# Kernel tuning notes

Measured on AMD Instinct MI355X. Metric: run time of the kernel, lower is better.

Reference implementation:

```python
import jax, jax.numpy as jnp
import numpy as np

N_NODES = 100000
N_EDGES = 1600000
N_FEAT = 16
HIDDEN = 128
N_GRAPHS = 512


def setup_inputs() -> dict:
    key = jax.random.key(0)
    ks = jax.random.split(key, 9)
    x = jax.random.normal(ks[0], (N_NODES, N_FEAT), dtype=jnp.float32)
    edge_index = jax.random.randint(ks[1], (2, N_EDGES), 0, N_NODES, dtype=jnp.int64)
    batch = jnp.sort(jax.random.randint(ks[2], (N_NODES,), 0, N_GRAPHS, dtype=jnp.int64))
    s1 = 1.0 / np.sqrt(N_FEAT)
    s2 = 1.0 / np.sqrt(HIDDEN)
    W1 = jax.random.uniform(ks[3], (N_FEAT, HIDDEN), jnp.float32, -s1, s1)
    b1 = jax.random.uniform(ks[4], (HIDDEN,), jnp.float32, -s1, s1)
    W2 = jax.random.uniform(ks[5], (HIDDEN, HIDDEN), jnp.float32, -s2, s2)
    b2 = jax.random.uniform(ks[6], (HIDDEN,), jnp.float32, -s2, s2)
    Wl = jax.random.uniform(ks[7], (HIDDEN, 1), jnp.float32, -s2, s2)
    bl = jax.random.uniform(ks[8], (1,), jnp.float32, -s2, s2)
    return {"x": x, "edge_index": edge_index, "batch": batch,
            "W1": W1, "b1": b1, "W2": W2, "b2": b2, "Wl": Wl, "bl": bl}


def _gcn_conv(x, W, b, src, dst, n_nodes):
    # PyG GCNConv: h = x @ W; add self-loops; sym-normalized scatter-add; + bias
    h = x @ W  # [N, H]
    deg = jnp.zeros((n_nodes,), h.dtype).at[dst].add(1.0) + 1.0  # self-loop adds 1
    dinv = jax.lax.rsqrt(deg)  # deg >= 1, safe
    norm = dinv[src] * dinv[dst]  # [E]
    out = jnp.zeros_like(h).at[dst].add(h[src] * norm[:, None])
    out = out + h * (dinv * dinv)[:, None]  # self-loop term
    return out + b


def reference(x, edge_index, batch, W1, b1, W2, b2, Wl, bl):
    src, dst = edge_index[0], edge_index[1]
    n = x.shape[0]
    h = jax.nn.relu(_gcn_conv(x, W1, b1, src, dst, n))
    h = jax.nn.relu(_gcn_conv(h, W2, b2, src, dst, n))
    # global_mean_pool over graphs
    sums = jax.ops.segment_sum(h, batch, num_segments=N_GRAPHS)
    counts = jax.ops.segment_sum(jnp.ones((n,), h.dtype), batch, num_segments=N_GRAPHS)
    pooled = sums / jnp.maximum(counts, 1.0)[:, None]  # [G, H]
    return (pooled @ Wl + bl).squeeze(-1)  # [G]
```

## Files before the change

kernel.cpp:

```cpp
#include <hip/hip_runtime.h>
#include <hip/hip_bf16.h>

#define N_NODES 100000
#define N_EDGES 1600000
#define N_FEAT  16
#define HIDDEN  128
#define N_GRAPHS 512
#define CAP     64
#define NBKT    782
#define BN      128
#define CAPB    2560
#define EPB     4000

typedef unsigned short ushort_t;
typedef short v8s __attribute__((ext_vector_type(8)));
typedef float v4f __attribute__((ext_vector_type(4)));

__device__ __forceinline__ ushort_t f2bf(float f) {
    __hip_bfloat16 b = __float2bfloat16(f);
    return *(ushort_t*)&b;
}
__device__ __forceinline__ float bf_lo(unsigned u) {
    union { unsigned i; float f; } c; c.i = u << 16; return c.f;
}
__device__ __forceinline__ float bf_hi(unsigned u) {
    union { unsigned i; float f; } c; c.i = u & 0xffff0000u; return c.f;
}


__global__ __launch_bounds__(256) void k_part(const int* __restrict__ src,
                                              const int* __restrict__ dst,
                                              int* __restrict__ bcnt,
                                              int* __restrict__ ebuf) {
    __shared__ int h[NBKT];
    __shared__ int base[NBKT];
    __shared__ int r[NBKT];
    int tid = threadIdx.x;
    int e0 = blockIdx.x * EPB;

    for (int i = tid; i < NBKT; i += 256) { h[i] = 0; r[i] = 0; }
    __syncthreads();

    int nloc = (tid < EPB - 15 * 256) ? 16 : 15;
    int v[16], bb[16];
    #pragma unroll
    for (int k = 0; k < 16; ++k) {
        if (k < nloc) {
            int i = e0 + tid + k * 256;
            int s = src[i], d = dst[i];
            bb[k] = d >> 7;
            v[k] = s | ((d & 127) << 17);
            atomicAdd(&h[bb[k]], 1);
        }
    }
    __syncthreads();

    for (int i = tid; i < NBKT; i += 256)
        base[i] = atomicAdd(&bcnt[i], h[i]);
    __syncthreads();

    #pragma unroll
    for (int k = 0; k < 16; ++k) {
        if (k < nloc) {
            int b = bb[k];
            int pos = base[b] + atomicAdd(&r[b], 1);
            if (pos < CAPB) ebuf[b * CAPB + pos] = v[k];
        }
    }
}


__global__ __launch_bounds__(256) void k_fill(const int* __restrict__ bcnt,
                                              const int* __restrict__ ebuf,
                                              int* __restrict__ esrc64,
                                              int* __restrict__ cnt,
                                              float* __restrict__ dinv) {
    __shared__ int lcnt[BN];
    int tid = threadIdx.x;
    int b = blockIdx.x;
    int node0 = b << 7;

    if (tid < BN) lcnt[tid] = 0;
    __syncthreads();

    int nE = bcnt[b]; nE = nE > CAPB ? CAPB : nE;
    const int* eb = ebuf + b * CAPB;
    for (int i = tid; i < nE; i += 256) {
        int v = eb[i];
        int dl = v >> 17;
        int p = atomicAdd(&lcnt[dl], 1);
        if (p < CAP) esrc64[((node0 + dl) << 6) + p] = v & 0x1FFFF;
    }
    __syncthreads();

    if (tid < BN) {
        int node = node0 + tid;
        if (node < N_NODES) {
            int c = lcnt[tid];
            cnt[node] = c;
            dinv[node] = rsqrtf((float)c + 1.0f);
            int cc = c > CAP ? CAP : c;
            int pad = (cc + 7) & ~7;
            for (int p = cc; p < pad; ++p)
                esrc64[(node << 6) + p] = N_NODES;
        }
    }
}


__global__ void k_prescale(const float* __restrict__ x, const float* __restrict__ dinv,
                           ushort_t* __restrict__ xb, ushort_t* __restrict__ h1) {
    int i = blockIdx.x * 256 + threadIdx.x;
    if (i < N_NODES * N_FEAT) {
        xb[i] = f2bf(x[i] * dinv[i >> 4]);
    } else if (i < (N_NODES + 1) * N_FEAT) {
        xb[i] = 0;
    } else if (i < (N_NODES + 1) * N_FEAT + HIDDEN) {
        h1[(size_t)N_NODES * HIDDEN + (i - (N_NODES + 1) * N_FEAT)] = 0;
    }
}


__global__ __launch_bounds__(256) void k_agg1f(const int* __restrict__ cnt,
                                               const int* __restrict__ esrc64,
                                               const float* __restrict__ dinv,
                                               const ushort_t* __restrict__ xb,
                                               const float* __restrict__ W1,
                                               const float* __restrict__ b1,
                                               ushort_t* __restrict__ h1) {
    __shared__ float sw[N_FEAT * HIDDEN];
    __shared__ float sx[32][20];
    __shared__ float sdd[32];
    int tid = threadIdx.x;
    for (int i = tid; i < N_FEAT * HIDDEN; i += 256) sw[i] = W1[i];

    int wv = tid >> 6;
    int sub = (tid >> 3) & 7;
    int l8 = tid & 7;
    int nl = wv * 8 + sub;
    int node = blockIdx.x * 32 + nl;
    const unsigned* xr = (const unsigned*)xb;

    int deg = cnt[node]; deg = deg > CAP ? CAP : deg;
    int deg8 = (deg + 7) & ~7;
    int base = node << 6;
    float dd = dinv[node];

    float a0 = 0.0f, a1 = 0.0f;
    for (int j = 0; j < deg8; j += 8) {
        int4 ia = *(const int4*)(esrc64 + base + j);
        int4 ib = *(const int4*)(esrc64 + base + j + 4);
        unsigned u0 = xr[(unsigned)ia.x * 8 + l8];
        unsigned u1 = xr[(unsigned)ia.y * 8 + l8];
        unsigned u2 = xr[(unsigned)ia.z * 8 + l8];
        unsigned u3 = xr[(unsigned)ia.w * 8 + l8];
        unsigned u4 = xr[(unsigned)ib.x * 8 + l8];
        unsigned u5 = xr[(unsigned)ib.y * 8 + l8];
        unsigned u6 = xr[(unsigned)ib.z * 8 + l8];
        unsigned u7 = xr[(unsigned)ib.w * 8 + l8];
        a0 += bf_lo(u0) + bf_lo(u1) + bf_lo(u2) + bf_lo(u3)
            + bf_lo(u4) + bf_lo(u5) + bf_lo(u6) + bf_lo(u7);
        a1 += bf_hi(u0) + bf_hi(u1) + bf_hi(u2) + bf_hi(u3)
            + bf_hi(u4) + bf_hi(u5) + bf_hi(u6) + bf_hi(u7);
    }
    unsigned su = xr[(unsigned)node * 8 + l8];
    a0 = (a0 + bf_lo(su)) * dd;
    a1 = (a1 + bf_hi(su)) * dd;

    sx[nl][2 * l8] = a0;
    sx[nl][2 * l8 + 1] = a1;
    if (l8 == 0) sdd[nl] = dd;
    __syncthreads();

    int f = tid & 127, half = tid >> 7;
    float bias = b1[f];
    float acc[16];
    #pragma unroll
    for (int n = 0; n < 16; ++n) acc[n] = bias;
    #pragma unroll
    for (int k4 = 0; k4 < 4; ++k4) {
        float w0 = sw[(k4 * 4 + 0) * HIDDEN + f];
        float w1 = sw[(k4 * 4 + 1) * HIDDEN + f];
        float w2 = sw[(k4 * 4 + 2) * HIDDEN + f];
        float w3 = sw[(k4 * 4 + 3) * HIDDEN + f];
        #pragma unroll
        for (int n = 0; n < 16; ++n) {
            float4 xv = *(const float4*)(&sx[half * 16 + n][k4 * 4]);
            acc[n] += xv.x * w0 + xv.y * w1 + xv.z * w2 + xv.w * w3;
        }
    }
    int n0 = blockIdx.x * 32 + half * 16;
    #pragma unroll
    for (int n = 0; n < 16; ++n)
        h1[(size_t)(n0 + n) * HIDDEN + f] =
            f2bf(sdd[half * 16 + n] * fmaxf(acc[n], 0.0f));
}


__global__ __launch_bounds__(256) void k_agg2(const int* __restrict__ cnt,
                                              const int* __restrict__ esrc64,
                                              const float* __restrict__ dinv,
                                              const ushort_t* __restrict__ h1,
                                              ushort_t* __restrict__ aggb) {
    int tid = threadIdx.x;
    int sub = tid >> 5;
    int l32 = tid & 31;
    int node = blockIdx.x * 8 + sub;
    const uint2* h = (const uint2*)h1;
    int deg = cnt[node]; deg = deg > CAP ? CAP : deg;
    int deg8 = (deg + 7) & ~7;
    int base = node << 6;
    float dd = dinv[node];

    uint2 sv = h[node * 32 + l32];
    float a0 = bf_lo(sv.x), a1 = bf_hi(sv.x), a2 = bf_lo(sv.y), a3 = bf_hi(sv.y);

    for (int j = 0; j < deg8; j += 8) {
        int4 ia = *(const int4*)(esrc64 + base + j);
        int4 ib = *(const int4*)(esrc64 + base + j + 4);
        uint2 v0 = h[(unsigned)ia.x * 32 + l32];
        uint2 v1 = h[(unsigned)ia.y * 32 + l32];
        uint2 v2 = h[(unsigned)ia.z * 32 + l32];
        uint2 v3 = h[(unsigned)ia.w * 32 + l32];
        uint2 v4 = h[(unsigned)ib.x * 32 + l32];
        uint2 v5 = h[(unsigned)ib.y * 32 + l32];
        uint2 v6 = h[(unsigned)ib.z * 32 + l32];
        uint2 v7 = h[(unsigned)ib.w * 32 + l32];
        a0 += bf_lo(v0.x) + bf_lo(v1.x) + bf_lo(v2.x) + bf_lo(v3.x)
            + bf_lo(v4.x) + bf_lo(v5.x) + bf_lo(v6.x) + bf_lo(v7.x);
        a1 += bf_hi(v0.x) + bf_hi(v1.x) + bf_hi(v2.x) + bf_hi(v3.x)
            + bf_hi(v4.x) + bf_hi(v5.x) + bf_hi(v6.x) + bf_hi(v7.x);
        a2 += bf_lo(v0.y) + bf_lo(v1.y) + bf_lo(v2.y) + bf_lo(v3.y)
            + bf_lo(v4.y) + bf_lo(v5.y) + bf_lo(v6.y) + bf_lo(v7.y);
        a3 += bf_hi(v0.y) + bf_hi(v1.y) + bf_hi(v2.y) + bf_hi(v3.y)
            + bf_hi(v4.y) + bf_hi(v5.y) + bf_hi(v6.y) + bf_hi(v7.y);
    }
    ushort4 r;
    r.x = f2bf(a0 * dd); r.y = f2bf(a1 * dd);
    r.z = f2bf(a2 * dd); r.w = f2bf(a3 * dd);
    ((ushort4*)aggb)[node * 32 + l32] = r;
}


__global__ void k_packB(const float* __restrict__ W2, ushort_t* __restrict__ Bp) {
    int idx = blockIdx.x * 256 + threadIdx.x;
    int j = idx & 7;
    int lane = (idx >> 3) & 63;
    int nt = (idx >> 9) & 7;
    int kt = idx >> 12;
    int k = kt * 32 + (lane >> 4) * 8 + j;
    int n = nt * 16 + (lane & 15);
    Bp[idx] = f2bf(W2[k * HIDDEN + n]);
}


__global__ __launch_bounds__(256) void k_mm2m(const ushort_t* __restrict__ A,
                                              const ushort_t* __restrict__ Bp,
                                              const float* __restrict__ b2,
                                              const float* __restrict__ Wl,
                                              float* __restrict__ snode) {
    __shared__ ushort_t sB[16384];
    int tid = threadIdx.x;
    {
        const uint4* s = (const uint4*)Bp;
        uint4* d = (uint4*)sB;
        #pragma unroll
        for (int j = 0; j < 8; ++j) d[tid + 256 * j] = s[tid + 256 * j];
    }
    __syncthreads();

    int wv = tid >> 6, lane = tid & 63;
    int m = lane & 15, quad = lane >> 4;
    int node0 = blockIdx.x * 64 + wv * 16;
    const ushort_t* arow = A + (size_t)(node0 + m) * HIDDEN;

    v4f acc[8];
    #pragma unroll
    for (int nt = 0; nt < 8; ++nt) acc[nt] = (v4f){0.f, 0.f, 0.f, 0.f};

    #pragma unroll
    for (int kt = 0; kt < 4; ++kt) {
        v8s a = *(const v8s*)(arow + kt * 32 + quad * 8);
        #pragma unroll
        for (int nt = 0; nt < 8; ++nt) {
            v8s b = *(const v8s*)(&sB[((kt * 8 + nt) * 64 + lane) * 8]);
            acc[nt] = __builtin_amdgcn_mfma_f32_16x16x32_bf16(a, b, acc[nt], 0, 0, 0);
        }
    }

    float part[4] = {0, 0, 0, 0};
    #pragma unroll
    for (int nt = 0; nt < 8; ++nt) {
        float bb = b2[nt * 16 + m];
        float wl = Wl[nt * 16 + m];
        #pragma unroll
        for (int reg = 0; reg < 4; ++reg)
            part[reg] += fmaxf(acc[nt][reg] + bb, 0.0f) * wl;
    }
    #pragma unroll
    for (int reg = 0; reg < 4; ++reg) {
        float p = part[reg];
        p += __shfl_xor(p, 1, 64);
        p += __shfl_xor(p, 2, 64);
        p += __shfl_xor(p, 4, 64);
        p += __shfl_xor(p, 8, 64);
        int node = node0 + quad * 4 + reg;
        if (m == 0 && node < N_NODES) snode[node] = p;
    }
}


__global__ __launch_bounds__(256) void k_pool(const float* __restrict__ snode,
                                              const int* __restrict__ batch,
                                              const float* __restrict__ bl,
                                              float* __restrict__ out) {
    int g = blockIdx.x;
    int tid = threadIdx.x;
    __shared__ float sred[4];

    int lo = 0, hi = N_NODES;
    while (lo < hi) { int mid = (lo + hi) >> 1; if (batch[mid] < g) lo = mid + 1; else hi = mid; }
    int start = lo;
    hi = N_NODES;
    while (lo < hi) { int mid = (lo + hi) >> 1; if (batch[mid] < g + 1) lo = mid + 1; else hi = mid; }
    int end = lo;

    float acc = 0.0f;
    for (int n = start + tid; n < end; n += 256) acc += snode[n];

    #pragma unroll
    for (int off = 32; off; off >>= 1) acc += __shfl_down(acc, off, 64);
    int wave = tid >> 6, lane = tid & 63;
    if (lane == 0) sred[wave] = acc;
    __syncthreads();
    if (tid == 0) {
        float s = sred[0] + sred[1] + sred[2] + sred[3];
        float cnt = (float)(end - start);
        out[g] = s / fmaxf(cnt, 1.0f) + bl[0];
    }
}


extern "C" void kernel_launch(void* const* d_in, const int* in_sizes, int n_in,
                              void* d_out, int out_size, void* d_ws, size_t ws_size,
                              hipStream_t stream) {
    const float* x    = (const float*)d_in[0];
    const int*   src  = (const int*)d_in[1];
    const int*   dst  = src + N_EDGES;
    const int*   batch= (const int*)d_in[2];
    const float* W1   = (const float*)d_in[3];
    const float* b1   = (const float*)d_in[4];
    const float* W2   = (const float*)d_in[5];
    const float* b2   = (const float*)d_in[6];
    const float* Wl   = (const float*)d_in[7];
    const float* bl   = (const float*)d_in[8];
    float* out = (float*)d_out;

    const size_t NH  = (size_t)N_NODES * HIDDEN;
    const size_t NH1 = (size_t)(N_NODES + 1) * HIDDEN;

    ushort_t* h1   = (ushort_t*)d_ws;
    ushort_t* aggb = h1 + NH1;
    int*   ebuf    = (int*)aggb;
    ushort_t* xb   = aggb + NH;
    float* dinv    = (float*)(xb + (size_t)(N_NODES + 1) * N_FEAT);
    float* snode   = dinv + N_NODES;
    int*   cnt     = (int*)(snode + N_NODES);
    int*   esrc64  = cnt + N_NODES;
    int*   bcnt    = esrc64 + (size_t)N_NODES * CAP;
    ushort_t* Bp   = (ushort_t*)(bcnt + NBKT);

    hipMemsetAsync(bcnt, 0, NBKT * sizeof(int), stream);
    k_part<<<N_EDGES / EPB, 256, 0, stream>>>(src, dst, bcnt, ebuf);
    k_fill<<<NBKT, 256, 0, stream>>>(bcnt, ebuf, esrc64, cnt, dinv);

    {
        int total = (N_NODES + 1) * N_FEAT + HIDDEN;
        k_prescale<<<(total + 255) / 256, 256, 0, stream>>>(x, dinv, xb, h1);
    }
    k_packB<<<64, 256, 0, stream>>>(W2, Bp);

    k_agg1f<<<N_NODES / 32, 256, 0, stream>>>(cnt, esrc64, dinv, xb, W1, b1, h1);

    k_agg2<<<N_NODES / 8, 256, 0, stream>>>(cnt, esrc64, dinv, h1, aggb);
    k_mm2m<<<(N_NODES + 63) / 64, 256, 0, stream>>>(aggb, Bp, b2, Wl, snode);

    k_pool<<<N_GRAPHS, 256, 0, stream>>>(snode, batch, bl, out);
}
```

Measured before the change: 231.9 us.

## Fuse layer-2 aggregation with MFMA matmul and fold small kernels into neighbors

Layer-2 gather aggregation now writes its bf16 rows into shared memory and feeds the MFMA matmul, bias, ReLU and Wl projection in the same kernel. This removes the aggb round trip through global memory and one launch. W2 packing is folded into extra blocks of the partition kernel, and x prescaling is folded into the fill kernel, cutting two more launches. In exchange, the fused kernel reads B fragments straight from global memory instead of staging them in LDS, and each block runs only 1563 blocks with 8 serial nodes per half-wave, which lowers parallelism for the gather.

```diff
diff --git a/kernel.cpp b/kernel.cpp
--- a/kernel.cpp
+++ b/kernel.cpp
@@ -31,11 +31,26 @@
 __global__ __launch_bounds__(256) void k_part(const int* __restrict__ src,
                                               const int* __restrict__ dst,
                                               int* __restrict__ bcnt,
-                                              int* __restrict__ ebuf) {
+                                              int* __restrict__ ebuf,
+                                              const float* __restrict__ W2,
+                                              ushort_t* __restrict__ Bp) {
+    int tid = threadIdx.x;
+
+    if (blockIdx.x >= N_EDGES / EPB) {
+        int idx = (blockIdx.x - N_EDGES / EPB) * 256 + tid;
+        int j = idx & 7;
+        int lane = (idx >> 3) & 63;
+        int nt = (idx >> 9) & 7;
+        int kt = idx >> 12;
+        int k = kt * 32 + (lane >> 4) * 8 + j;
+        int n = nt * 16 + (lane & 15);
+        Bp[idx] = f2bf(W2[k * HIDDEN + n]);
+        return;
+    }
+
     __shared__ int h[NBKT];
     __shared__ int base[NBKT];
     __shared__ int r[NBKT];
-    int tid = threadIdx.x;
     int e0 = blockIdx.x * EPB;
 
     for (int i = tid; i < NBKT; i += 256) { h[i] = 0; r[i] = 0; }
@@ -72,9 +87,12 @@
 
 __global__ __launch_bounds__(256) void k_fill(const int* __restrict__ bcnt,
                                               const int* __restrict__ ebuf,
+                                              const float* __restrict__ x,
                                               int* __restrict__ esrc64,
                                               int* __restrict__ cnt,
-                                              float* __restrict__ dinv) {
+                                              float* __restrict__ dinv,
+                                              ushort_t* __restrict__ xb,
+                                              ushort_t* __restrict__ h1) {
     __shared__ int lcnt[BN];
     int tid = threadIdx.x;
     int b = blockIdx.x;
@@ -105,18 +123,19 @@
                 esrc64[(node << 6) + p] = N_NODES;
         }
     }
-}
-
-
-__global__ void k_prescale(const float* __restrict__ x, const float* __restrict__ dinv,
-                           ushort_t* __restrict__ xb, ushort_t* __restrict__ h1) {
-    int i = blockIdx.x * 256 + threadIdx.x;
-    if (i < N_NODES * N_FEAT) {
-        xb[i] = f2bf(x[i] * dinv[i >> 4]);
-    } else if (i < (N_NODES + 1) * N_FEAT) {
-        xb[i] = 0;
-    } else if (i < (N_NODES + 1) * N_FEAT + HIDDEN) {
-        h1[(size_t)N_NODES * HIDDEN + (i - (N_NODES + 1) * N_FEAT)] = 0;
+
+    for (int i = tid; i < BN * N_FEAT; i += 256) {
+        int nl = i >> 4;
+        int node = node0 + nl;
+        if (node < N_NODES) {
+            float di = rsqrtf((float)lcnt[nl] + 1.0f);
+            xb[node * N_FEAT + (i & 15)] = f2bf(x[node * N_FEAT + (i & 15)] * di);
+        }
+    }
+
+    if (b == 0) {
+        if (tid < N_FEAT) xb[N_NODES * N_FEAT + tid] = 0;
+        if (tid < HIDDEN) h1[(size_t)N_NODES * HIDDEN + tid] = 0;
     }
 }
 
@@ -197,82 +216,61 @@
 }
 
 
-__global__ __launch_bounds__(256) void k_agg2(const int* __restrict__ cnt,
-                                              const int* __restrict__ esrc64,
-                                              const float* __restrict__ dinv,
-                                              const ushort_t* __restrict__ h1,
-                                              ushort_t* __restrict__ aggb) {
-    int tid = threadIdx.x;
-    int sub = tid >> 5;
-    int l32 = tid & 31;
-    int node = blockIdx.x * 8 + sub;
+__global__ __launch_bounds__(256) void k_l2(const int* __restrict__ cnt,
+                                            const int* __restrict__ esrc64,
+                                            const float* __restrict__ dinv,
+                                            const ushort_t* __restrict__ h1,
+                                            const ushort_t* __restrict__ Bp,
+                                            const float* __restrict__ b2,
+                                            const float* __restrict__ Wl,
+                                            float* __restrict__ snode) {
+    __shared__ ushort_t sA[64 * 132];
+    int tid = threadIdx.x;
+    int wv = tid >> 6, lane = tid & 63;
+    int half = lane >> 5, l32 = lane & 31;
+    int node0 = blockIdx.x * 64;
     const uint2* h = (const uint2*)h1;
-    int deg = cnt[node]; deg = deg > CAP ? CAP : deg;
-    int deg8 = (deg + 7) & ~7;
-    int base = node << 6;
-    float dd = dinv[node];
-
-    uint2 sv = h[node * 32 + l32];
-    float a0 = bf_lo(sv.x), a1 = bf_hi(sv.x), a2 = bf_lo(sv.y), a3 = bf_hi(sv.y);
-
-    for (int j = 0; j < deg8; j += 8) {
-        int4 ia = *(const int4*)(esrc64 + base + j);
-        int4 ib = *(const int4*)(esrc64 + base + j + 4);
-        uint2 v0 = h[(unsigned)ia.x * 32 + l32];
-        uint2 v1 = h[(unsigned)ia.y * 32 + l32];
-        uint2 v2 = h[(unsigned)ia.z * 32 + l32];
-        uint2 v3 = h[(unsigned)ia.w * 32 + l32];
-        uint2 v4 = h[(unsigned)ib.x * 32 + l32];
-        uint2 v5 = h[(unsigned)ib.y * 32 + l32];
-        uint2 v6 = h[(unsigned)ib.z * 32 + l32];
-        uint2 v7 = h[(unsigned)ib.w * 32 + l32];
-        a0 += bf_lo(v0.x) + bf_lo(v1.x) + bf_lo(v2.x) + bf_lo(v3.x)
-            + bf_lo(v4.x) + bf_lo(v5.x) + bf_lo(v6.x) + bf_lo(v7.x);
-        a1 += bf_hi(v0.x) + bf_hi(v1.x) + bf_hi(v2.x) + bf_hi(v3.x)
-            + bf_hi(v4.x) + bf_hi(v5.x) + bf_hi(v6.x) + bf_hi(v7.x);
-        a2 += bf_lo(v0.y) + bf_lo(v1.y) + bf_lo(v2.y) + bf_lo(v3.y)
-            + bf_lo(v4.y) + bf_lo(v5.y) + bf_lo(v6.y) + bf_lo(v7.y);
-        a3 += bf_hi(v0.y) + bf_hi(v1.y) + bf_hi(v2.y) + bf_hi(v3.y)
-            + bf_hi(v4.y) + bf_hi(v5.y) + bf_hi(v6.y) + bf_hi(v7.y);
-    }
-    ushort4 r;
-    r.x = f2bf(a0 * dd); r.y = f2bf(a1 * dd);
-    r.z = f2bf(a2 * dd); r.w = f2bf(a3 * dd);
-    ((ushort4*)aggb)[node * 32 + l32] = r;
-}
-
-
-__global__ void k_packB(const float* __restrict__ W2, ushort_t* __restrict__ Bp) {
-    int idx = blockIdx.x * 256 + threadIdx.x;
-    int j = idx & 7;
-    int lane = (idx >> 3) & 63;
-    int nt = (idx >> 9) & 7;
-    int kt = idx >> 12;
-    int k = kt * 32 + (lane >> 4) * 8 + j;
-    int n = nt * 16 + (lane & 15);
-    Bp[idx] = f2bf(W2[k * HIDDEN + n]);
-}
-
-
-__global__ __launch_bounds__(256) void k_mm2m(const ushort_t* __restrict__ A,
-                                              const ushort_t* __restrict__ Bp,
-                                              const float* __restrict__ b2,
-                                              const float* __restrict__ Wl,
-                                              float* __restrict__ snode) {
-    __shared__ ushort_t sB[16384];
-    int tid = threadIdx.x;
-    {
-        const uint4* s = (const uint4*)Bp;
-        uint4* d = (uint4*)sB;
-        #pragma unroll
-        for (int j = 0; j < 8; ++j) d[tid + 256 * j] = s[tid + 256 * j];
-    }
-    __syncthreads();
-
-    int wv = tid >> 6, lane = tid & 63;
+
+    for (int p = 0; p < 8; ++p) {
+        int nl = wv * 16 + p * 2 + half;
+        int node = node0 + nl;
+        bool valid = node < N_NODES;
+        int deg = valid ? cnt[node] : 0; deg = deg > CAP ? CAP : deg;
+        int deg8 = (deg + 7) & ~7;
+        int base = node << 6;
+        float dd = valid ? dinv[node] : 0.0f;
+        uint2 sv = valid ? h[node * 32 + l32] : (uint2){0u, 0u};
+        float a0 = bf_lo(sv.x), a1 = bf_hi(sv.x), a2 = bf_lo(sv.y), a3 = bf_hi(sv.y);
+
+        for (int j = 0; j < deg8; j += 8) {
+            int4 ia = *(const int4*)(esrc64 + base + j);
+            int4 ib = *(const int4*)(esrc64 + base + j + 4);
+            uint2 v0 = h[(unsigned)ia.x * 32 + l32];
+            uint2 v1 = h[(unsigned)ia.y * 32 + l32];
+            uint2 v2 = h[(unsigned)ia.z * 32 + l32];
+            uint2 v3 = h[(unsigned)ia.w * 32 + l32];
+            uint2 v4 = h[(unsigned)ib.x * 32 + l32];
+            uint2 v5 = h[(unsigned)ib.y * 32 + l32];
+            uint2 v6 = h[(unsigned)ib.z * 32 + l32];
+            uint2 v7 = h[(unsigned)ib.w * 32 + l32];
+            a0 += bf_lo(v0.x) + bf_lo(v1.x) + bf_lo(v2.x) + bf_lo(v3.x)
+                + bf_lo(v4.x) + bf_lo(v5.x) + bf_lo(v6.x) + bf_lo(v7.x);
+            a1 += bf_hi(v0.x) + bf_hi(v1.x) + bf_hi(v2.x) + bf_hi(v3.x)
+                + bf_hi(v4.x) + bf_hi(v5.x) + bf_hi(v6.x) + bf_hi(v7.x);
+            a2 += bf_lo(v0.y) + bf_lo(v1.y) + bf_lo(v2.y) + bf_lo(v3.y)
+                + bf_lo(v4.y) + bf_lo(v5.y) + bf_lo(v6.y) + bf_lo(v7.y);
+            a3 += bf_hi(v0.y) + bf_hi(v1.y) + bf_hi(v2.y) + bf_hi(v3.y)
+                + bf_hi(v4.y) + bf_hi(v5.y) + bf_hi(v6.y) + bf_hi(v7.y);
+        }
+        ushort4 r;
+        r.x = f2bf(a0 * dd); r.y = f2bf(a1 * dd);
+        r.z = f2bf(a2 * dd); r.w = f2bf(a3 * dd);
+        *(ushort4*)(&sA[nl * 132 + l32 * 4]) = r;
+    }
+    __syncthreads();
+
     int m = lane & 15, quad = lane >> 4;
-    int node0 = blockIdx.x * 64 + wv * 16;
-    const ushort_t* arow = A + (size_t)(node0 + m) * HIDDEN;
+    const ushort_t* arow = &sA[(wv * 16 + m) * 132];
 
     v4f acc[8];
     #pragma unroll
@@ -280,11 +278,13 @@
 
     #pragma unroll
     for (int kt = 0; kt < 4; ++kt) {
-        v8s a = *(const v8s*)(arow + kt * 32 + quad * 8);
+        union { v8s v; ushort4 q[2]; } au;
+        au.q[0] = *(const ushort4*)(arow + kt * 32 + quad * 8);
+        au.q[1] = *(const ushort4*)(arow + kt * 32 + quad * 8 + 4);
         #pragma unroll
         for (int nt = 0; nt < 8; ++nt) {
-            v8s b = *(const v8s*)(&sB[((kt * 8 + nt) * 64 + lane) * 8]);
-            acc[nt] = __builtin_amdgcn_mfma_f32_16x16x32_bf16(a, b, acc[nt], 0, 0, 0);
+            v8s b = *(const v8s*)(Bp + ((kt * 8 + nt) * 64 + lane) * 8);
+            acc[nt] = __builtin_amdgcn_mfma_f32_16x16x32_bf16(au.v, b, acc[nt], 0, 0, 0);
         }
     }
 
@@ -297,6 +297,7 @@
         for (int reg = 0; reg < 4; ++reg)
             part[reg] += fmaxf(acc[nt][reg] + bb, 0.0f) * wl;
     }
+    int node0b = node0 + wv * 16;
     #pragma unroll
     for (int reg = 0; reg < 4; ++reg) {
         float p = part[reg];
@@ -304,7 +305,7 @@
         p += __shfl_xor(p, 2, 64);
         p += __shfl_xor(p, 4, 64);
         p += __shfl_xor(p, 8, 64);
-        int node = node0 + quad * 4 + reg;
+        int node = node0b + quad * 4 + reg;
         if (m == 0 && node < N_NODES) snode[node] = p;
     }
 }
@@ -356,34 +357,27 @@
     const float* bl   = (const float*)d_in[8];
     float* out = (float*)d_out;
 
-    const size_t NH  = (size_t)N_NODES * HIDDEN;
-    const size_t NH1 = (size_t)(N_NODES + 1) * HIDDEN;
-
-    ushort_t* h1   = (ushort_t*)d_ws;
-    ushort_t* aggb = h1 + NH1;
-    int*   ebuf    = (int*)aggb;
-    ushort_t* xb   = aggb + NH;
-    float* dinv    = (float*)(xb + (size_t)(N_NODES + 1) * N_FEAT);
-    float* snode   = dinv + N_NODES;
-    int*   cnt     = (int*)(snode + N_NODES);
-    int*   esrc64  = cnt + N_NODES;
-    int*   bcnt    = esrc64 + (size_t)N_NODES * CAP;
-    ushort_t* Bp   = (ushort_t*)(bcnt + NBKT);
+    char* w = (char*)d_ws;
+    size_t off = 0;
+    auto alloc = [&](size_t bytes) { char* p = w + off; off = (off + bytes + 255) & ~(size_t)255; return p; };
+
+    ushort_t* h1   = (ushort_t*)alloc((size_t)(N_NODES + 1) * HIDDEN * 2);
+    int*   ebuf    = (int*)alloc((size_t)NBKT * CAPB * 4);
+    ushort_t* xb   = (ushort_t*)alloc((size_t)(N_NODES + 1) * N_FEAT * 2);
+    float* dinv    = (float*)alloc(N_NODES * 4);
+    float* snode   = (float*)alloc(N_NODES * 4);
+    int*   cnt     = (int*)alloc(N_NODES * 4);
+    int*   esrc64  = (int*)alloc((size_t)N_NODES * CAP * 4);
+    ushort_t* Bp   = (ushort_t*)alloc(16384 * 2);
+    int*   bcnt    = (int*)alloc(NBKT * 4);
 
     hipMemsetAsync(bcnt, 0, NBKT * sizeof(int), stream);
-    k_part<<<N_EDGES / EPB, 256, 0, stream>>>(src, dst, bcnt, ebuf);
-    k_fill<<<NBKT, 256, 0, stream>>>(bcnt, ebuf, esrc64, cnt, dinv);
-
-    {
-        int total = (N_NODES + 1) * N_FEAT + HIDDEN;
-        k_prescale<<<(total + 255) / 256, 256, 0, stream>>>(x, dinv, xb, h1);
-    }
-    k_packB<<<64, 256, 0, stream>>>(W2, Bp);
+    k_part<<<N_EDGES / EPB + 64, 256, 0, stream>>>(src, dst, bcnt, ebuf, W2, Bp);
+    k_fill<<<NBKT, 256, 0, stream>>>(bcnt, ebuf, x, esrc64, cnt, dinv, xb, h1);
 
     k_agg1f<<<N_NODES / 32, 256, 0, stream>>>(cnt, esrc64, dinv, xb, W1, b1, h1);
 
-    k_agg2<<<N_NODES / 8, 256, 0, stream>>>(cnt, esrc64, dinv, h1, aggb);
-    k_mm2m<<<(N_NODES + 63) / 64, 256, 0, stream>>>(aggb, Bp, b2, Wl, snode);
+    k_l2<<<(N_NODES + 63) / 64, 256, 0, stream>>>(cnt, esrc64, dinv, h1, Bp, b2, Wl, snode);
 
     k_pool<<<N_GRAPHS, 256, 0, stream>>>(snode, batch, bl, out);
 }
```

After: 227.9 us. Within noise of the previous version (-1.7%).
